# Kernel tuning notes

Measured on AMD Instinct MI355X. Metric: run time of the kernel, lower is better.

The kernel has to match this reference:

```python
import jax, jax.numpy as jnp
import numpy as np

N, DIM, HID, E = 100000, 128, 512, 600000


def setup_inputs() -> dict:
    key = jax.random.key(0)
    k_h, k_src, k_dst, k_w1, k_b1, k_w2, k_b2 = jax.random.split(key, 7)
    h = jax.random.normal(k_h, (N, DIM), dtype=jnp.float32)
    src = jax.random.randint(k_src, (E,), 0, N)
    dst = jax.random.randint(k_dst, (E,), 0, N)
    edge_index = jnp.stack([src, dst], axis=0).astype(jnp.int64)
    # Linear params stored as [in, out] (math-equivalent to torch's [out,in].T)
    s1 = 1.0 / np.sqrt(2 * DIM)
    s2 = 1.0 / np.sqrt(HID)
    W1 = jax.random.uniform(k_w1, (2 * DIM, HID), jnp.float32, -s1, s1)
    b1 = jax.random.uniform(k_b1, (HID,), jnp.float32, -s1, s1)
    W2 = jax.random.uniform(k_w2, (HID, DIM), jnp.float32, -s2, s2)
    b2 = jax.random.uniform(k_b2, (DIM,), jnp.float32, -s2, s2)
    return {"h": h, "edge_index": edge_index, "W1": W1, "b1": b1, "W2": W2, "b2": b2}


def reference(h, edge_index, W1, b1, W2, b2):
    src, dst = edge_index[0], edge_index[1]
    n = h.shape[0]
    # scatter-mean: sum gathered neighbor features per destination node
    agg_sum = jax.ops.segment_sum(h[src], dst, num_segments=n)  # [N, DIM]
    deg = jax.ops.segment_sum(jnp.ones((src.shape[0],), h.dtype), dst, num_segments=n)  # [N]
    mean = agg_sum / jnp.maximum(deg, 1.0)[:, None]
    # isolated nodes (deg==0) fall back to their own features
    agg = jnp.where((deg == 0)[:, None], h, mean)
    x = jnp.concatenate([h, agg], axis=-1)  # [N, 2*DIM]
    hdn = jax.nn.gelu(x @ W1 + b1, approximate=False)  # torch GELU default = exact erf
    return hdn @ W2 + b2
```

## Files before the change

kernel.cpp:

```cpp
#include <hip/hip_runtime.h>
#include <hip/hip_bf16.h>
#include <math.h>

#define N_NODES 100000
#define DIM 128
#define HID 512
#define EDGES 600000
#define SCAN_CHUNK 1024
#define SCAN_NBLK ((N_NODES + SCAN_CHUNK - 1) / SCAN_CHUNK)
#define MROWS_PAD 100096

typedef short bf16x8 __attribute__((ext_vector_type(8)));
typedef float f32x4 __attribute__((ext_vector_type(4)));


__device__ inline unsigned short f32_to_bf16(float f) {
    unsigned int u = __float_as_uint(f);
    u += 0x7fff + ((u >> 16) & 1);
    return (unsigned short)(u >> 16);
}

__device__ inline float gelu_f(float x) {
    float x3 = x * x * x;
    float y = 0.7978845608028654f * x + 0.0356774081f * x3;
    float e = exp2f(y * 2.8853900817779268f);
    float t = 1.0f - 2.0f * __builtin_amdgcn_rcpf(e + 1.0f);
    return 0.5f * x * (1.0f + t);
}

__device__ inline void gload16(const void* g, void* l) {
    __builtin_amdgcn_global_load_lds(
        (const __attribute__((address_space(1))) unsigned int*)g,
        (__attribute__((address_space(3))) unsigned int*)l,
        16, 0, 0);
}

#define PREP_W1_BLKS 512
#define PREP_W2_BLKS 128
#define PREP_CONV_BLKS 12500
#define PREP_COUNT_BLKS ((EDGES + 255) / 256)
#define PREP_TOTAL (PREP_W1_BLKS + PREP_W2_BLKS + PREP_CONV_BLKS + PREP_COUNT_BLKS)

__global__ __launch_bounds__(256) void mgl_prep_kernel(
    const float* __restrict__ h, const int* __restrict__ ei,
    const float* __restrict__ W1, const float* __restrict__ W2,
    unsigned short* __restrict__ X, unsigned short* __restrict__ W1T,
    unsigned short* __restrict__ W2T, int* __restrict__ cnt)
{
    int b = blockIdx.x;
    if (b < PREP_W1_BLKS) {
        int n = b;
        int k = threadIdx.x;
        unsigned short val = f32_to_bf16(W1[(size_t)k * HID + n]);
        int byteoff = (k * 2) ^ ((n & 7) << 4);
        *(unsigned short*)((char*)(W1T + (size_t)n * 256) + byteoff) = val;
        return;
    }
    b -= PREP_W1_BLKS;
    if (b < PREP_W2_BLKS) {
        int n = b;
        #pragma unroll
        for (int it = 0; it < 2; ++it) {
            int k = threadIdx.x + it * 256;
            unsigned short val = f32_to_bf16(W2[(size_t)k * DIM + n]);
            int byteoff = (k * 2) ^ ((n & 7) << 4);
            *(unsigned short*)((char*)(W2T + (size_t)n * 512) + byteoff) = val;
        }
        return;
    }
    b -= PREP_W2_BLKS;
    if (b < PREP_CONV_BLKS) {
        int t = b * 256 + threadIdx.x;
        if (t >= N_NODES * (DIM / 4)) return;
        int node = t >> 5;
        int c4 = t & 31;
        float4 v = *(const float4*)(h + (size_t)node * DIM + c4 * 4);
        ushort4 p;
        p.x = f32_to_bf16(v.x); p.y = f32_to_bf16(v.y);
        p.z = f32_to_bf16(v.z); p.w = f32_to_bf16(v.w);
        int byteoff = (c4 * 8) ^ ((node & 7) << 4);
        *(ushort4*)((char*)(X + (size_t)node * 256) + byteoff) = p;
        return;
    }
    b -= PREP_CONV_BLKS;
    {
        int e = b * 256 + threadIdx.x;
        if (e < EDGES) atomicAdd(&cnt[ei[EDGES + e]], 1);
    }
}

__global__ __launch_bounds__(256) void mgl_scan_block_kernel(
    const int* __restrict__ cnt, int* __restrict__ row_start, int* __restrict__ bsum)
{
    __shared__ int sdata[256];
    int t = threadIdx.x;
    int base = blockIdx.x * SCAN_CHUNK + t * 4;
    int v[4];
    #pragma unroll
    for (int i = 0; i < 4; ++i) {
        int idx = base + i;
        v[i] = (idx < N_NODES) ? cnt[idx] : 0;
    }
    int tsum = v[0] + v[1] + v[2] + v[3];
    sdata[t] = tsum;
    __syncthreads();
    for (int off = 1; off < 256; off <<= 1) {
        int x = (t >= off) ? sdata[t - off] : 0;
        __syncthreads();
        sdata[t] += x;
        __syncthreads();
    }
    int run = (t > 0) ? sdata[t - 1] : 0;
    #pragma unroll
    for (int i = 0; i < 4; ++i) {
        int idx = base + i;
        if (idx < N_NODES) row_start[idx] = run;
        run += v[i];
    }
    if (t == 255) bsum[blockIdx.x] = sdata[255];
}

__global__ __launch_bounds__(128) void mgl_scan_bsum_kernel(int* __restrict__ bsum)
{
    __shared__ int sd[128];
    int t = threadIdx.x;
    int v = (t < SCAN_NBLK) ? bsum[t] : 0;
    sd[t] = v;
    __syncthreads();
    for (int off = 1; off < 128; off <<= 1) {
        int x = (t >= off) ? sd[t - off] : 0;
        __syncthreads();
        sd[t] += x;
        __syncthreads();
    }
    if (t < SCAN_NBLK) bsum[t] = sd[t] - v;
}

__global__ __launch_bounds__(256) void mgl_scan_add_kernel(
    int* __restrict__ row_start, const int* __restrict__ bsum)
{
    int i = blockIdx.x * 256 + threadIdx.x;
    if (i < N_NODES) row_start[i] += bsum[i / SCAN_CHUNK];
    if (i == 0) row_start[N_NODES] = EDGES;
}

__global__ __launch_bounds__(256) void mgl_fill_kernel(
    const int* __restrict__ ei, const int* __restrict__ row_start,
    int* __restrict__ cnt, int* __restrict__ csr)
{
    int e = blockIdx.x * 256 + threadIdx.x;
    if (e >= EDGES) return;
    int s = ei[e];
    int t = ei[EDGES + e];
    int pos = atomicSub(&cnt[t], 1) - 1;
    csr[row_start[t] + pos] = s;
}

__global__ __launch_bounds__(256) void mgl_gather_mean_kernel(
    const unsigned short* __restrict__ Xb, const int* __restrict__ row_start,
    const int* __restrict__ csr, unsigned short* __restrict__ X)
{
    int v = blockIdx.x * 4 + (threadIdx.x >> 6);
    if (v >= N_NODES) return;
    int lane = threadIdx.x & 63;
    int beg = row_start[v];
    int nb = row_start[v + 1] - beg;
    int laneByte = lane * 4;
    const char* xb = (const char*)Xb;

    if (nb > 0) {
        float2 acc = make_float2(0.f, 0.f);
        for (int base = 0; base < nb; base += 64) {
            int rem = nb - base; if (rem > 64) rem = 64;
            int sv = (lane < rem) ? csr[beg + base + lane] : 0;
            for (int j = 0; j < rem; ++j) {
                int s = __shfl(sv, j);
                unsigned int pk = *(const unsigned int*)(
                    xb + (size_t)s * 512 + (laneByte ^ ((s & 7) << 4)));
                acc.x += __uint_as_float(pk << 16);
                acc.y += __uint_as_float(pk & 0xffff0000u);
            }
        }
        float inv = 1.f / (float)nb;
        unsigned int po = (unsigned int)f32_to_bf16(acc.x * inv) |
                          ((unsigned int)f32_to_bf16(acc.y * inv) << 16);
        *(unsigned int*)((char*)(X + (size_t)v * 256) +
                         ((256 + laneByte) ^ ((v & 7) << 4))) = po;
    } else {
        unsigned int pk = *(const unsigned int*)(
            xb + (size_t)v * 512 + (laneByte ^ ((v & 7) << 4)));
        *(unsigned int*)((char*)(X + (size_t)v * 256) +
                         ((256 + laneByte) ^ ((v & 7) << 4))) = pk;
    }
}

template<int KTOT, int NI, int NGROUPS, int PARTS, bool GELU_OUT>
__global__ __launch_bounds__(512) void mgl_mlp_kernel(
    const unsigned short* __restrict__ Wt,
    const unsigned short* __restrict__ Xr,
    const float* __restrict__ bias,
    void* __restrict__ outp)
{
    constexpr int NT = KTOT / 64;
    constexpr int KB = KTOT * 2;
    constexpr int WROWS = NI * 32;
    constexpr int SHIFT = (NT == 4) ? 2 : 3;
    constexpr int TILES = MROWS_PAD / 256;

    __shared__ char lds[65536 + 2 * 32768];
    char* ldsW = lds;
    char* ldsX = lds + 65536;

    int tid = threadIdx.x;
    int w = tid >> 6, l = tid & 63;

    int vbid = ((blockIdx.x & 7) << 5) + (blockIdx.x >> 3);
    int p = vbid / NGROUPS;
    int ng = vbid % NGROUPS;
    int T = (TILES - p + PARTS - 1) / PARTS;
    int C = T << SHIFT;

    int wm = w >> 1, wn = w & 1;
    int r16 = l & 15, kq = l >> 4;
    int rowmask = (r16 & 7) << 4;

    {
        const char* wg = (const char*)Wt + (size_t)ng * WROWS * KB;
        #pragma unroll
        for (int i = 0; i < 8; ++i) {
            int byte = i * 8192 + tid * 16;
            int row = byte / KB, col = byte & (KB - 1);
            gload16(wg + (size_t)row * KB + col, ldsW + byte);
        }
    }
    {
        int m0 = p * 256;
        #pragma unroll
        for (int i = 0; i < 4; ++i) {
            int byte = i * 8192 + tid * 16;
            int row = byte >> 7, col = byte & 127;
            gload16((const char*)Xr + (size_t)(m0 + row) * KB + col, ldsX + byte);
        }
    }

    f32x4 acc[4][NI] = {};

    for (int c = 0; c < C; ++c) {
        int kt = c & (NT - 1);
        char* bufc = ldsX + (c & 1) * 32768;
        if (c + 1 < C) {
            int c2 = c + 1;
            int kt2 = c2 & (NT - 1);
            int m02 = (p + (c2 >> SHIFT) * PARTS) * 256;
            char* bufn = ldsX + (c2 & 1) * 32768;
            #pragma unroll
            for (int i = 0; i < 4; ++i) {
                int byte = i * 8192 + tid * 16;
                int row = byte >> 7, col = byte & 127;
                gload16((const char*)Xr + (size_t)(m02 + row) * KB + kt2 * 128 + col,
                        bufn + byte);
            }
            asm volatile("s_waitcnt vmcnt(4)" ::: "memory");
        } else {
            asm volatile("s_waitcnt vmcnt(0)" ::: "memory");
        }
        __builtin_amdgcn_s_barrier();

        #pragma unroll
        for (int kk = 0; kk < 2; ++kk) {
            int posb = (kk * 64 + kq * 16) ^ rowmask;
            bf16x8 a[NI], b[4];
            #pragma unroll
            for (int ni = 0; ni < NI; ++ni)
                a[ni] = *(const bf16x8*)(ldsW +
                    (size_t)(wn * (NI * 16) + ni * 16 + r16) * KB + kt * 128 + posb);
            #pragma unroll
            for (int mi = 0; mi < 4; ++mi)
                b[mi] = *(const bf16x8*)(bufc + (wm * 64 + mi * 16 + r16) * 128 + posb);
            #pragma unroll
            for (int mi = 0; mi < 4; ++mi)
                #pragma unroll
                for (int ni = 0; ni < NI; ++ni)
                    acc[mi][ni] = __builtin_amdgcn_mfma_f32_16x16x32_bf16(
                        a[ni], b[mi], acc[mi][ni], 0, 0, 0);
        }
        __builtin_amdgcn_s_barrier();

        if (kt == NT - 1) {
            int m0 = (p + (c >> SHIFT) * PARTS) * 256;
            #pragma unroll
            for (int mi = 0; mi < 4; ++mi) {
                int m = m0 + wm * 64 + mi * 16 + r16;
                #pragma unroll
                for (int ni = 0; ni < NI; ++ni) {
                    int nc = ng * (NI * 32) + wn * (NI * 16) + ni * 16 + kq * 4;
                    float4 bv = *(const float4*)(bias + nc);
                    float x0 = acc[mi][ni][0] + bv.x;
                    float x1 = acc[mi][ni][1] + bv.y;
                    float x2 = acc[mi][ni][2] + bv.z;
                    float x3 = acc[mi][ni][3] + bv.w;
                    if (GELU_OUT) {
                        ushort4 pk;
                        pk.x = f32_to_bf16(gelu_f(x0));
                        pk.y = f32_to_bf16(gelu_f(x1));
                        pk.z = f32_to_bf16(gelu_f(x2));
                        pk.w = f32_to_bf16(gelu_f(x3));
                        unsigned short* row = (unsigned short*)outp + (size_t)m * HID;
                        int byteoff = (nc * 2) ^ ((m & 7) << 4);
                        *(ushort4*)((char*)row + byteoff) = pk;
                    } else if (m < N_NODES) {
                        float4 o = make_float4(x0, x1, x2, x3);
                        *(float4*)((float*)outp + (size_t)m * DIM + nc) = o;
                    }
                    acc[mi][ni] = (f32x4){0.f, 0.f, 0.f, 0.f};
                }
            }
        }
    }
}

extern "C" void kernel_launch(void* const* d_in, const int* in_sizes, int n_in,
                              void* d_out, int out_size, void* d_ws, size_t ws_size,
                              hipStream_t stream) {
    const float* h  = (const float*)d_in[0];
    const int*   ei = (const int*)d_in[1];
    const float* W1 = (const float*)d_in[2];
    const float* b1 = (const float*)d_in[3];
    const float* W2 = (const float*)d_in[4];
    const float* b2 = (const float*)d_in[5];
    float* out = (float*)d_out;

    unsigned short* X   = (unsigned short*)d_ws;
    unsigned short* hdn = X + (size_t)MROWS_PAD * 256;
    unsigned short* W1T = hdn + (size_t)MROWS_PAD * 512;
    unsigned short* W2T = W1T + 512 * 256;
    int* cnt = (int*)(W2T + 128 * 512);
    int* row_start = cnt + N_NODES;
    int* bsum = row_start + N_NODES + 1;
    int* csr = bsum + 128;

    hipMemsetAsync(cnt, 0, N_NODES * sizeof(int), stream);
    mgl_prep_kernel<<<PREP_TOTAL, 256, 0, stream>>>(h, ei, W1, W2, X, W1T, W2T, cnt);
    mgl_scan_block_kernel<<<SCAN_NBLK, 256, 0, stream>>>(cnt, row_start, bsum);
    mgl_scan_bsum_kernel<<<1, 128, 0, stream>>>(bsum);
    mgl_scan_add_kernel<<<(N_NODES + 255) / 256, 256, 0, stream>>>(row_start, bsum);
    mgl_fill_kernel<<<(EDGES + 255) / 256, 256, 0, stream>>>(ei, row_start, cnt, csr);
    mgl_gather_mean_kernel<<<(N_NODES + 3) / 4, 256, 0, stream>>>(X, row_start, csr, X);

    mgl_mlp_kernel<256, 4, 4, 64, true><<<256, 512, 0, stream>>>(W1T, X, b1, hdn);
    mgl_mlp_kernel<512, 2, 2, 128, false><<<256, 512, 0, stream>>>(W2T, hdn, b2, out);
}
```

Before: 233.3 us.

## Fuse both MLP GEMMs into one kernel keeping hidden activations in LDS

Replaces the two persistent MLP GEMM kernels with one fused kernel. Each block owns 64 rows, holds the X tile in registers, streams W1 then W2 tiles through a four-slot LDS ring, and keeps the GELU hidden tile in LDS. This removes the global round trip of the bf16 hidden matrix and one launch. In exchange every block re-streams the full weights, the grid grows to about 1564 blocks, and 128KB of LDS per block limits occupancy.

```diff
diff --git a/kernel.cpp b/kernel.cpp
--- a/kernel.cpp
+++ b/kernel.cpp
@@ -194,127 +194,175 @@
     }
 }
 
-template<int KTOT, int NI, int NGROUPS, int PARTS, bool GELU_OUT>
-__global__ __launch_bounds__(512) void mgl_mlp_kernel(
-    const unsigned short* __restrict__ Wt,
+__global__ __launch_bounds__(512) void mgl_fused_mlp_kernel(
+    const unsigned short* __restrict__ W1T,
+    const unsigned short* __restrict__ W2T,
     const unsigned short* __restrict__ Xr,
-    const float* __restrict__ bias,
-    void* __restrict__ outp)
-{
-    constexpr int NT = KTOT / 64;
-    constexpr int KB = KTOT * 2;
-    constexpr int WROWS = NI * 32;
-    constexpr int SHIFT = (NT == 4) ? 2 : 3;
-    constexpr int TILES = MROWS_PAD / 256;
-
-    __shared__ char lds[65536 + 2 * 32768];
-    char* ldsW = lds;
-    char* ldsX = lds + 65536;
-
-    int tid = threadIdx.x;
-    int w = tid >> 6, l = tid & 63;
-
-    int vbid = ((blockIdx.x & 7) << 5) + (blockIdx.x >> 3);
-    int p = vbid / NGROUPS;
-    int ng = vbid % NGROUPS;
-    int T = (TILES - p + PARTS - 1) / PARTS;
-    int C = T << SHIFT;
-
-    int wm = w >> 1, wn = w & 1;
-    int r16 = l & 15, kq = l >> 4;
-    int rowmask = (r16 & 7) << 4;
-
-    {
-        const char* wg = (const char*)Wt + (size_t)ng * WROWS * KB;
-        #pragma unroll
-        for (int i = 0; i < 8; ++i) {
-            int byte = i * 8192 + tid * 16;
-            int row = byte / KB, col = byte & (KB - 1);
-            gload16(wg + (size_t)row * KB + col, ldsW + byte);
-        }
-    }
-    {
-        int m0 = p * 256;
-        #pragma unroll
-        for (int i = 0; i < 4; ++i) {
-            int byte = i * 8192 + tid * 16;
-            int row = byte >> 7, col = byte & 127;
-            gload16((const char*)Xr + (size_t)(m0 + row) * KB + col, ldsX + byte);
-        }
-    }
-
-    f32x4 acc[4][NI] = {};
-
-    for (int c = 0; c < C; ++c) {
-        int kt = c & (NT - 1);
-        char* bufc = ldsX + (c & 1) * 32768;
-        if (c + 1 < C) {
-            int c2 = c + 1;
-            int kt2 = c2 & (NT - 1);
-            int m02 = (p + (c2 >> SHIFT) * PARTS) * 256;
-            char* bufn = ldsX + (c2 & 1) * 32768;
-            #pragma unroll
-            for (int i = 0; i < 4; ++i) {
-                int byte = i * 8192 + tid * 16;
-                int row = byte >> 7, col = byte & 127;
-                gload16((const char*)Xr + (size_t)(m02 + row) * KB + kt2 * 128 + col,
-                        bufn + byte);
-            }
-            asm volatile("s_waitcnt vmcnt(4)" ::: "memory");
-        } else {
-            asm volatile("s_waitcnt vmcnt(0)" ::: "memory");
-        }
+    const float* __restrict__ b1f, const float* __restrict__ b2f,
+    float* __restrict__ outp)
+{
+    __shared__ char lds[131072];
+    char* ring = lds;
+    char* hdnl = lds + 65536;
+
+    const int tid = threadIdx.x;
+    const int w = tid >> 6, l = tid & 63;
+    const int wm = w >> 2, wn = w & 3;
+    const int r16 = l & 15, kq = l >> 4;
+    const int rowmask = (r16 & 7) << 4;
+    const int m0 = blockIdx.x * 64;
+
+    float4 b1v[4][2], b2v[2];
+    #pragma unroll
+    for (int ng = 0; ng < 4; ++ng)
+        #pragma unroll
+        for (int ni = 0; ni < 2; ++ni)
+            b1v[ng][ni] = *(const float4*)(b1f + ng * 128 + wn * 32 + ni * 16 + kq * 4);
+    #pragma unroll
+    for (int ni = 0; ni < 2; ++ni)
+        b2v[ni] = *(const float4*)(b2f + wn * 32 + ni * 16 + kq * 4);
+
+    bf16x8 xf[2][4][2];
+    #pragma unroll
+    for (int mi = 0; mi < 2; ++mi) {
+        int m = m0 + wm * 32 + mi * 16 + r16;
+        const char* xrow = (const char*)Xr + (size_t)m * 512;
+        int swz = (m & 7) << 4;
+        #pragma unroll
+        for (int kt = 0; kt < 4; ++kt)
+            #pragma unroll
+            for (int kk = 0; kk < 2; ++kk)
+                xf[mi][kt][kk] = *(const bf16x8*)(
+                    xrow + ((kt * 128 + kk * 64 + kq * 16) ^ swz));
+    }
+    asm volatile("s_waitcnt vmcnt(0)" ::: "memory");
+
+    auto stageW1 = [&](int slot, int ng, int kt) {
+        #pragma unroll
+        for (int i = 0; i < 2; ++i) {
+            int c = w + i * 8;
+            int row = c * 8 + (l >> 3);
+            int col = (l & 7) * 16;
+            const char* g = (const char*)W1T +
+                (size_t)(ng * 128 + row) * 512 + kt * 128 + col;
+            gload16(g, ring + slot * 16384 + c * 1024 + l * 16);
+        }
+    };
+    auto stageW2 = [&](int slot, int kt) {
+        #pragma unroll
+        for (int i = 0; i < 2; ++i) {
+            int c = w + i * 8;
+            int row = c * 8 + (l >> 3);
+            int col = (l & 7) * 16;
+            const char* g = (const char*)W2T +
+                (size_t)row * 1024 + kt * 128 + col;
+            gload16(g, ring + slot * 16384 + c * 1024 + l * 16);
+        }
+    };
+
+    stageW1(0, 0, 0);
+    stageW1(1, 0, 1);
+    stageW1(2, 0, 2);
+
+    f32x4 acc[2][2] = {};
+
+    #pragma unroll
+    for (int s = 0; s < 16; ++s) {
+        asm volatile("s_waitcnt vmcnt(4)" ::: "memory");
         __builtin_amdgcn_s_barrier();
 
+        const int ng = s >> 2, kt = s & 3;
+        const char* wbase = ring + (s & 3) * 16384;
         #pragma unroll
         for (int kk = 0; kk < 2; ++kk) {
-            int posb = (kk * 64 + kq * 16) ^ rowmask;
-            bf16x8 a[NI], b[4];
-            #pragma unroll
-            for (int ni = 0; ni < NI; ++ni)
-                a[ni] = *(const bf16x8*)(ldsW +
-                    (size_t)(wn * (NI * 16) + ni * 16 + r16) * KB + kt * 128 + posb);
-            #pragma unroll
-            for (int mi = 0; mi < 4; ++mi)
-                b[mi] = *(const bf16x8*)(bufc + (wm * 64 + mi * 16 + r16) * 128 + posb);
-            #pragma unroll
-            for (int mi = 0; mi < 4; ++mi)
+            bf16x8 a[2];
+            #pragma unroll
+            for (int ni = 0; ni < 2; ++ni)
+                a[ni] = *(const bf16x8*)(wbase +
+                    (wn * 32 + ni * 16 + r16) * 128 + ((kk * 64 + kq * 16) ^ rowmask));
+            #pragma unroll
+            for (int mi = 0; mi < 2; ++mi)
                 #pragma unroll
-                for (int ni = 0; ni < NI; ++ni)
+                for (int ni = 0; ni < 2; ++ni)
                     acc[mi][ni] = __builtin_amdgcn_mfma_f32_16x16x32_bf16(
-                        a[ni], b[mi], acc[mi][ni], 0, 0, 0);
-        }
-        __builtin_amdgcn_s_barrier();
-
-        if (kt == NT - 1) {
-            int m0 = (p + (c >> SHIFT) * PARTS) * 256;
-            #pragma unroll
-            for (int mi = 0; mi < 4; ++mi) {
-                int m = m0 + wm * 64 + mi * 16 + r16;
+                        a[ni], xf[mi][kt][kk], acc[mi][ni], 0, 0, 0);
+        }
+
+        {
+            const int sg = s + 3;
+            if (sg < 16) stageW1(sg & 3, sg >> 2, sg & 3);
+            else         stageW2(sg & 3, sg - 16);
+        }
+
+        if (kt == 3) {
+            #pragma unroll
+            for (int mi = 0; mi < 2; ++mi) {
+                int ml = wm * 32 + mi * 16 + r16;
+                int mswz = (ml & 7) << 4;
                 #pragma unroll
-                for (int ni = 0; ni < NI; ++ni) {
-                    int nc = ng * (NI * 32) + wn * (NI * 16) + ni * 16 + kq * 4;
-                    float4 bv = *(const float4*)(bias + nc);
-                    float x0 = acc[mi][ni][0] + bv.x;
-                    float x1 = acc[mi][ni][1] + bv.y;
-                    float x2 = acc[mi][ni][2] + bv.z;
-                    float x3 = acc[mi][ni][3] + bv.w;
-                    if (GELU_OUT) {
-                        ushort4 pk;
-                        pk.x = f32_to_bf16(gelu_f(x0));
-                        pk.y = f32_to_bf16(gelu_f(x1));
-                        pk.z = f32_to_bf16(gelu_f(x2));
-                        pk.w = f32_to_bf16(gelu_f(x3));
-                        unsigned short* row = (unsigned short*)outp + (size_t)m * HID;
-                        int byteoff = (nc * 2) ^ ((m & 7) << 4);
-                        *(ushort4*)((char*)row + byteoff) = pk;
-                    } else if (m < N_NODES) {
-                        float4 o = make_float4(x0, x1, x2, x3);
-                        *(float4*)((float*)outp + (size_t)m * DIM + nc) = o;
-                    }
+                for (int ni = 0; ni < 2; ++ni) {
+                    int ncl = ng * 128 + wn * 32 + ni * 16 + kq * 4;
+                    float4 bv = b1v[ng][ni];
+                    ushort4 pk;
+                    pk.x = f32_to_bf16(gelu_f(acc[mi][ni][0] + bv.x));
+                    pk.y = f32_to_bf16(gelu_f(acc[mi][ni][1] + bv.y));
+                    pk.z = f32_to_bf16(gelu_f(acc[mi][ni][2] + bv.z));
+                    pk.w = f32_to_bf16(gelu_f(acc[mi][ni][3] + bv.w));
+                    *(ushort4*)(hdnl + ml * 1024 + ((ncl * 2) ^ mswz)) = pk;
                     acc[mi][ni] = (f32x4){0.f, 0.f, 0.f, 0.f};
                 }
             }
+        }
+    }
+
+    asm volatile("s_waitcnt lgkmcnt(0)" ::: "memory");
+    __builtin_amdgcn_s_barrier();
+
+    f32x4 acc2[2][2] = {};
+    #pragma unroll
+    for (int s2 = 0; s2 < 8; ++s2) {
+        if (s2 < 6)      asm volatile("s_waitcnt vmcnt(4)" ::: "memory");
+        else if (s2 == 6) asm volatile("s_waitcnt vmcnt(2)" ::: "memory");
+        else              asm volatile("s_waitcnt vmcnt(0)" ::: "memory");
+        __builtin_amdgcn_s_barrier();
+
+        const char* wbase = ring + (s2 & 3) * 16384;
+        #pragma unroll
+        for (int kk = 0; kk < 2; ++kk) {
+            bf16x8 a[2], b[2];
+            #pragma unroll
+            for (int ni = 0; ni < 2; ++ni)
+                a[ni] = *(const bf16x8*)(wbase +
+                    (wn * 32 + ni * 16 + r16) * 128 + ((kk * 64 + kq * 16) ^ rowmask));
+            #pragma unroll
+            for (int mi = 0; mi < 2; ++mi) {
+                int ml = wm * 32 + mi * 16 + r16;
+                b[mi] = *(const bf16x8*)(hdnl + ml * 1024 +
+                    ((s2 * 128 + kk * 64 + kq * 16) ^ ((ml & 7) << 4)));
+            }
+            #pragma unroll
+            for (int mi = 0; mi < 2; ++mi)
+                #pragma unroll
+                for (int ni = 0; ni < 2; ++ni)
+                    acc2[mi][ni] = __builtin_amdgcn_mfma_f32_16x16x32_bf16(
+                        a[ni], b[mi], acc2[mi][ni], 0, 0, 0);
+        }
+        if (s2 + 3 < 8) stageW2((s2 + 3) & 3, s2 + 3);
+    }
+
+    #pragma unroll
+    for (int mi = 0; mi < 2; ++mi) {
+        int m = m0 + wm * 32 + mi * 16 + r16;
+        if (m >= N_NODES) continue;
+        #pragma unroll
+        for (int ni = 0; ni < 2; ++ni) {
+            int nc = wn * 32 + ni * 16 + kq * 4;
+            float4 o;
+            o.x = acc2[mi][ni][0] + b2v[ni].x;
+            o.y = acc2[mi][ni][1] + b2v[ni].y;
+            o.z = acc2[mi][ni][2] + b2v[ni].z;
+            o.w = acc2[mi][ni][3] + b2v[ni].w;
+            *(float4*)(outp + (size_t)m * DIM + nc) = o;
         }
     }
 }
@@ -331,8 +379,7 @@
     float* out = (float*)d_out;
 
     unsigned short* X   = (unsigned short*)d_ws;
-    unsigned short* hdn = X + (size_t)MROWS_PAD * 256;
-    unsigned short* W1T = hdn + (size_t)MROWS_PAD * 512;
+    unsigned short* W1T = X + (size_t)MROWS_PAD * 256;
     unsigned short* W2T = W1T + 512 * 256;
     int* cnt = (int*)(W2T + 128 * 512);
     int* row_start = cnt + N_NODES;
@@ -347,6 +394,5 @@
     mgl_fill_kernel<<<(EDGES + 255) / 256, 256, 0, stream>>>(ei, row_start, cnt, csr);
     mgl_gather_mean_kernel<<<(N_NODES + 3) / 4, 256, 0, stream>>>(X, row_start, csr, X);
 
-    mgl_mlp_kernel<256, 4, 4, 64, true><<<256, 512, 0, stream>>>(W1T, X, b1, hdn);
-    mgl_mlp_kernel<512, 2, 2, 128, false><<<256, 512, 0, stream>>>(W2T, hdn, b2, out);
-}
+    mgl_fused_mlp_kernel<<<MROWS_PAD / 64, 512, 0, stream>>>(W1T, W2T, X, b1, b2, out);
+}
```

Result: faster. 227.8 us (-2.3%).

## Hold MLP weights in registers and stream contiguous row chunks with triple buffering

Applied to the files above, without the earlier changes.

Replaces the templated LDS-weight GEMM with two specialized kernels. Each wave keeps its full slice of W1 or W2 in VGPRs, so only activation rows go through LDS, loaded as contiguous 32KB chunks (64 rows for layer 1, 32 rows for layer 2) with a three-slot prefetch ring. Every block now produces all output columns of its rows, which removes the N-group split that made each X tile be read by several blocks. In exchange it uses many more registers per wave (128 VGPRs of weights in layer 1), which may limit occupancy or cause spills, and it keeps only 256 blocks.

```diff
diff --git a/kernel.cpp b/kernel.cpp
--- a/kernel.cpp
+++ b/kernel.cpp
@@ -9,6 +9,8 @@
 #define SCAN_CHUNK 1024
 #define SCAN_NBLK ((N_NODES + SCAN_CHUNK - 1) / SCAN_CHUNK)
 #define MROWS_PAD 100096
+#define NCH1 (MROWS_PAD / 64)
+#define NCH2 (MROWS_PAD / 32)
 
 typedef short bf16x8 __attribute__((ext_vector_type(8)));
 typedef float f32x4 __attribute__((ext_vector_type(4)));
@@ -194,126 +196,159 @@
     }
 }
 
-template<int KTOT, int NI, int NGROUPS, int PARTS, bool GELU_OUT>
-__global__ __launch_bounds__(512) void mgl_mlp_kernel(
-    const unsigned short* __restrict__ Wt,
+__global__ __launch_bounds__(512, 2) void mgl_mlp1_kernel(
+    const unsigned short* __restrict__ W1T,
     const unsigned short* __restrict__ Xr,
-    const float* __restrict__ bias,
-    void* __restrict__ outp)
-{
-    constexpr int NT = KTOT / 64;
-    constexpr int KB = KTOT * 2;
-    constexpr int WROWS = NI * 32;
-    constexpr int SHIFT = (NT == 4) ? 2 : 3;
-    constexpr int TILES = MROWS_PAD / 256;
-
-    __shared__ char lds[65536 + 2 * 32768];
-    char* ldsW = lds;
-    char* ldsX = lds + 65536;
-
-    int tid = threadIdx.x;
-    int w = tid >> 6, l = tid & 63;
-
-    int vbid = ((blockIdx.x & 7) << 5) + (blockIdx.x >> 3);
-    int p = vbid / NGROUPS;
-    int ng = vbid % NGROUPS;
-    int T = (TILES - p + PARTS - 1) / PARTS;
-    int C = T << SHIFT;
-
-    int wm = w >> 1, wn = w & 1;
-    int r16 = l & 15, kq = l >> 4;
-    int rowmask = (r16 & 7) << 4;
-
+    const float* __restrict__ b1f,
+    unsigned short* __restrict__ hdn)
+{
+    __shared__ char ldsX[3 * 32768];
+    const int tid = threadIdx.x;
+    const int w = tid >> 6, l = tid & 63;
+    const int r16 = l & 15, kq = l >> 4;
+    const int rmask = (r16 & 7) << 4;
+    const int n0w = w * 64;
+
+    bf16x8 a1[4][8];
+    #pragma unroll
+    for (int nb = 0; nb < 4; ++nb) {
+        const char* wrow = (const char*)W1T + (size_t)(n0w + nb * 16 + r16) * 512;
+        #pragma unroll
+        for (int ks = 0; ks < 8; ++ks)
+            a1[nb][ks] = *(const bf16x8*)(wrow + ((ks * 64 + kq * 16) ^ rmask));
+    }
+    float4 b1v[4];
+    #pragma unroll
+    for (int nb = 0; nb < 4; ++nb)
+        b1v[nb] = *(const float4*)(b1f + n0w + nb * 16 + kq * 4);
+
+    const int bid = blockIdx.x;
+    const int nch = (NCH1 - bid + 255) >> 8;
+
+    auto stage = [&](int slot, int cj) {
+        const char* src = (const char*)Xr + (size_t)cj * 32768;
+        char* dst = ldsX + slot * 32768;
+        #pragma unroll
+        for (int i = 0; i < 4; ++i) {
+            int off = i * 8192 + tid * 16;
+            gload16(src + off, dst + off);
+        }
+    };
+
+    stage(0, bid);
+    if (nch > 1) stage(1, bid + 256);
+
+    for (int j = 0; j < nch; ++j) {
+        asm volatile("s_waitcnt vmcnt(4)" ::: "memory");
+        __builtin_amdgcn_s_barrier();
+        asm volatile("" ::: "memory");
+        if (j + 2 < nch) stage((j + 2) % 3, bid + (j + 2) * 256);
+
+        const char* bX = ldsX + (j % 3) * 32768;
+        f32x4 acc[4][4] = {};
+        #pragma unroll
+        for (int ks = 0; ks < 8; ++ks) {
+            bf16x8 b[4];
+            #pragma unroll
+            for (int mb = 0; mb < 4; ++mb)
+                b[mb] = *(const bf16x8*)(bX + (mb * 16 + r16) * 512 +
+                                         ((ks * 64 + kq * 16) ^ rmask));
+            #pragma unroll
+            for (int mb = 0; mb < 4; ++mb)
+                #pragma unroll
+                for (int nb = 0; nb < 4; ++nb)
+                    acc[mb][nb] = __builtin_amdgcn_mfma_f32_16x16x32_bf16(
+                        a1[nb][ks], b[mb], acc[mb][nb], 0, 0, 0);
+        }
+
+        const size_t m0c = (size_t)(bid + j * 256) * 64;
+        #pragma unroll
+        for (int mb = 0; mb < 4; ++mb) {
+            size_t m = m0c + mb * 16 + r16;
+            char* hrow = (char*)hdn + m * 1024;
+            #pragma unroll
+            for (int nb = 0; nb < 4; ++nb) {
+                int nc = n0w + nb * 16 + kq * 4;
+                ushort4 pk;
+                pk.x = f32_to_bf16(gelu_f(acc[mb][nb][0] + b1v[nb].x));
+                pk.y = f32_to_bf16(gelu_f(acc[mb][nb][1] + b1v[nb].y));
+                pk.z = f32_to_bf16(gelu_f(acc[mb][nb][2] + b1v[nb].z));
+                pk.w = f32_to_bf16(gelu_f(acc[mb][nb][3] + b1v[nb].w));
+                *(ushort4*)(hrow + ((nc * 2) ^ rmask)) = pk;
+            }
+        }
+    }
+}
+
+__global__ __launch_bounds__(512, 2) void mgl_mlp2_kernel(
+    const unsigned short* __restrict__ W2T,
+    const unsigned short* __restrict__ hdn,
+    const float* __restrict__ b2f,
+    float* __restrict__ outp)
+{
+    __shared__ char ldsH[3 * 32768];
+    const int tid = threadIdx.x;
+    const int w = tid >> 6, l = tid & 63;
+    const int r16 = l & 15, kq = l >> 4;
+    const int rmask = (r16 & 7) << 4;
+
+    bf16x8 a2[16];
     {
-        const char* wg = (const char*)Wt + (size_t)ng * WROWS * KB;
-        #pragma unroll
-        for (int i = 0; i < 8; ++i) {
-            int byte = i * 8192 + tid * 16;
-            int row = byte / KB, col = byte & (KB - 1);
-            gload16(wg + (size_t)row * KB + col, ldsW + byte);
-        }
-    }
-    {
-        int m0 = p * 256;
+        const char* wrow = (const char*)W2T + (size_t)(w * 16 + r16) * 1024;
+        #pragma unroll
+        for (int ks = 0; ks < 16; ++ks)
+            a2[ks] = *(const bf16x8*)(wrow + ((ks * 64 + kq * 16) ^ rmask));
+    }
+    float4 b2v = *(const float4*)(b2f + w * 16 + kq * 4);
+
+    const int bid = blockIdx.x;
+    const int nch = (NCH2 - bid + 255) >> 8;
+
+    auto stage = [&](int slot, int cj) {
+        const char* src = (const char*)hdn + (size_t)cj * 32768;
+        char* dst = ldsH + slot * 32768;
         #pragma unroll
         for (int i = 0; i < 4; ++i) {
-            int byte = i * 8192 + tid * 16;
-            int row = byte >> 7, col = byte & 127;
-            gload16((const char*)Xr + (size_t)(m0 + row) * KB + col, ldsX + byte);
-        }
-    }
-
-    f32x4 acc[4][NI] = {};
-
-    for (int c = 0; c < C; ++c) {
-        int kt = c & (NT - 1);
-        char* bufc = ldsX + (c & 1) * 32768;
-        if (c + 1 < C) {
-            int c2 = c + 1;
-            int kt2 = c2 & (NT - 1);
-            int m02 = (p + (c2 >> SHIFT) * PARTS) * 256;
-            char* bufn = ldsX + (c2 & 1) * 32768;
-            #pragma unroll
-            for (int i = 0; i < 4; ++i) {
-                int byte = i * 8192 + tid * 16;
-                int row = byte >> 7, col = byte & 127;
-                gload16((const char*)Xr + (size_t)(m02 + row) * KB + kt2 * 128 + col,
-                        bufn + byte);
-            }
-            asm volatile("s_waitcnt vmcnt(4)" ::: "memory");
-        } else {
-            asm volatile("s_waitcnt vmcnt(0)" ::: "memory");
-        }
+            int off = i * 8192 + tid * 16;
+            gload16(src + off, dst + off);
+        }
+    };
+
+    stage(0, bid);
+    if (nch > 1) stage(1, bid + 256);
+
+    for (int j = 0; j < nch; ++j) {
+        asm volatile("s_waitcnt vmcnt(4)" ::: "memory");
         __builtin_amdgcn_s_barrier();
-
-        #pragma unroll
-        for (int kk = 0; kk < 2; ++kk) {
-            int posb = (kk * 64 + kq * 16) ^ rowmask;
-            bf16x8 a[NI], b[4];
-            #pragma unroll
-            for (int ni = 0; ni < NI; ++ni)
-                a[ni] = *(const bf16x8*)(ldsW +
-                    (size_t)(wn * (NI * 16) + ni * 16 + r16) * KB + kt * 128 + posb);
-            #pragma unroll
-            for (int mi = 0; mi < 4; ++mi)
-                b[mi] = *(const bf16x8*)(bufc + (wm * 64 + mi * 16 + r16) * 128 + posb);
-            #pragma unroll
-            for (int mi = 0; mi < 4; ++mi)
-                #pragma unroll
-                for (int ni = 0; ni < NI; ++ni)
-                    acc[mi][ni] = __builtin_amdgcn_mfma_f32_16x16x32_bf16(
-                        a[ni], b[mi], acc[mi][ni], 0, 0, 0);
-        }
-        __builtin_amdgcn_s_barrier();
-
-        if (kt == NT - 1) {
-            int m0 = (p + (c >> SHIFT) * PARTS) * 256;
-            #pragma unroll
-            for (int mi = 0; mi < 4; ++mi) {
-                int m = m0 + wm * 64 + mi * 16 + r16;
-                #pragma unroll
-                for (int ni = 0; ni < NI; ++ni) {
-                    int nc = ng * (NI * 32) + wn * (NI * 16) + ni * 16 + kq * 4;
-                    float4 bv = *(const float4*)(bias + nc);
-                    float x0 = acc[mi][ni][0] + bv.x;
-                    float x1 = acc[mi][ni][1] + bv.y;
-                    float x2 = acc[mi][ni][2] + bv.z;
-                    float x3 = acc[mi][ni][3] + bv.w;
-                    if (GELU_OUT) {
-                        ushort4 pk;
-                        pk.x = f32_to_bf16(gelu_f(x0));
-                        pk.y = f32_to_bf16(gelu_f(x1));
-                        pk.z = f32_to_bf16(gelu_f(x2));
-                        pk.w = f32_to_bf16(gelu_f(x3));
-                        unsigned short* row = (unsigned short*)outp + (size_t)m * HID;
-                        int byteoff = (nc * 2) ^ ((m & 7) << 4);
-                        *(ushort4*)((char*)row + byteoff) = pk;
-                    } else if (m < N_NODES) {
-                        float4 o = make_float4(x0, x1, x2, x3);
-                        *(float4*)((float*)outp + (size_t)m * DIM + nc) = o;
-                    }
-                    acc[mi][ni] = (f32x4){0.f, 0.f, 0.f, 0.f};
-                }
+        asm volatile("" ::: "memory");
+        if (j + 2 < nch) stage((j + 2) % 3, bid + (j + 2) * 256);
+
+        const char* bH = ldsH + (j % 3) * 32768;
+        f32x4 acc[2] = {};
+        #pragma unroll
+        for (int ks = 0; ks < 16; ++ks) {
+            bf16x8 b[2];
+            #pragma unroll
+            for (int mb = 0; mb < 2; ++mb)
+                b[mb] = *(const bf16x8*)(bH + (mb * 16 + r16) * 1024 +
+                                         ((ks * 64 + kq * 16) ^ rmask));
+            #pragma unroll
+            for (int mb = 0; mb < 2; ++mb)
+                acc[mb] = __builtin_amdgcn_mfma_f32_16x16x32_bf16(
+                    a2[ks], b[mb], acc[mb], 0, 0, 0);
+        }
+
+        const size_t m0c = (size_t)(bid + j * 256) * 32;
+        #pragma unroll
+        for (int mb = 0; mb < 2; ++mb) {
+            size_t m = m0c + mb * 16 + r16;
+            if (m < N_NODES) {
+                float4 o;
+                o.x = acc[mb][0] + b2v.x;
+                o.y = acc[mb][1] + b2v.y;
+                o.z = acc[mb][2] + b2v.z;
+                o.w = acc[mb][3] + b2v.w;
+                *(float4*)(outp + m * DIM + w * 16 + kq * 4) = o;
             }
         }
     }
@@ -347,6 +382,6 @@
     mgl_fill_kernel<<<(EDGES + 255) / 256, 256, 0, stream>>>(ei, row_start, cnt, csr);
     mgl_gather_mean_kernel<<<(N_NODES + 3) / 4, 256, 0, stream>>>(X, row_start, csr, X);
 
-    mgl_mlp_kernel<256, 4, 4, 64, true><<<256, 512, 0, stream>>>(W1T, X, b1, hdn);
-    mgl_mlp_kernel<512, 2, 2, 128, false><<<256, 512, 0, stream>>>(W2T, hdn, b2, out);
-}
+    mgl_mlp1_kernel<<<256, 512, 0, stream>>>(W1T, X, b1, hdn);
+    mgl_mlp2_kernel<<<256, 512, 0, stream>>>(W2T, hdn, b2, out);
+}
```

Measured after the change: 224.4 us. 1.04x faster.
